# Kernel tuning notes

Hardware: AMD Instinct MI355X
Metric: run time of the kernel (lower is better)

The kernel has to match this reference:

```python
import jax, jax.numpy as jnp
import numpy as np

N_LAYERS, K, EPS = 3, 3, 1e-5
N, E, IN_CH, HID, OUT_CH = 50000, 800000, 16, 64, 4


def setup_inputs() -> dict:
    key = jax.random.key(0)
    ks = jax.random.split(key, 10)
    x = jax.random.normal(ks[0], (N, IN_CH), jnp.float32)
    edge_index = jax.random.randint(ks[1], (2, E), 0, N, dtype=jnp.int32)
    batch = jnp.zeros((N,), jnp.int32)  # unused by forward, kept for signature parity
    W_in = jax.random.normal(ks[2], (IN_CH, HID), jnp.float32) / np.sqrt(IN_CH)
    b_in = jnp.zeros((HID,), jnp.float32)
    cheb_W = jax.random.normal(ks[3], (N_LAYERS, K, HID, HID), jnp.float32) / np.sqrt(HID)
    cheb_b = jnp.zeros((N_LAYERS, HID), jnp.float32)
    ln_g = jnp.ones((N_LAYERS, HID), jnp.float32)
    ln_b = jnp.zeros((N_LAYERS, HID), jnp.float32)
    W_out = jax.random.normal(ks[4], (HID, OUT_CH), jnp.float32) / np.sqrt(HID)
    b_out = jnp.zeros((OUT_CH,), jnp.float32)
    return dict(x=x, edge_index=edge_index, batch=batch, W_in=W_in, b_in=b_in,
                cheb_W=cheb_W, cheb_b=cheb_b, ln_g=ln_g, ln_b=ln_b,
                W_out=W_out, b_out=b_out)


def _layernorm(h, g, b):
    mu = h.mean(-1, keepdims=True)
    var = ((h - mu) ** 2).mean(-1, keepdims=True)
    return (h - mu) * jax.lax.rsqrt(var + EPS) * g + b


def reference(x, edge_index, batch, W_in, b_in, cheb_W, cheb_b, ln_g, ln_b, W_out, b_out):
    n = x.shape[0]
    src, dst = edge_index[0], edge_index[1]
    # PyG ChebConv sym norm with lambda_max=2: L_hat = -D^{-1/2} A D^{-1/2}, zero diagonal
    deg = jax.ops.segment_sum(jnp.ones_like(src, x.dtype), src, num_segments=n)
    dinv = jnp.where(deg > 0, 1.0 / jnp.sqrt(jnp.maximum(deg, 1.0)), 0.0)
    w = -dinv[src] * dinv[dst]  # [E]

    def prop(h):  # h: [N, H] -> L_hat @ h via gather/scatter over edges
        return jax.ops.segment_sum(w[:, None] * h[src], dst, num_segments=n)

    h = x @ W_in + b_in
    for i in range(N_LAYERS):
        identity = h
        Tx0 = h
        out = Tx0 @ cheb_W[i, 0]
        Tx1 = prop(Tx0)
        out = out + Tx1 @ cheb_W[i, 1]
        for k in range(2, K):
            Tx2 = 2.0 * prop(Tx1) - Tx0
            out = out + Tx2 @ cheb_W[i, k]
            Tx0, Tx1 = Tx1, Tx2
        h = jax.nn.relu(out + cheb_b[i])  # dropout inactive (eval)
        h = h + identity
        h = _layernorm(h, ln_g[i], ln_b[i])
    return h @ W_out + b_out
```

## Files before the change

### kernel.cpp

```cpp
#include <hip/hip_runtime.h>
#include <hip/hip_bf16.h>

#define HID 64
#define CAP 64
#define LDK 200
#define Q4W 6272
typedef __hip_bfloat16 bf16;
typedef __attribute__((ext_vector_type(8))) short short8x;
typedef __attribute__((ext_vector_type(4))) float f32x4;

__device__ __forceinline__ float ldf(const void* p, int i, int bf) {
    return bf ? __bfloat162float(((const bf16*)p)[i]) : ((const float*)p)[i];
}
__device__ __forceinline__ unsigned short f2u16(float f) {
    bf16 h = __float2bfloat16(f);
    return *(unsigned short*)&h;
}
__device__ __forceinline__ float u162f(unsigned short u) {
    return __bfloat162float(*(const bf16*)&u);
}
__device__ __forceinline__ unsigned int pack2(float a, float b) {
    return (unsigned int)f2u16(a) | ((unsigned int)f2u16(b) << 16);
}
__device__ __forceinline__ unsigned int t3w(unsigned int t2w, unsigned int hw) {
    float a = 2.f * __uint_as_float(t2w << 16) - __uint_as_float(hw << 16);
    float b = 2.f * __uint_as_float(t2w & 0xffff0000u) - __uint_as_float(hw & 0xffff0000u);
    return pack2(a, b);
}
__device__ __forceinline__ void accum8(float* acc, uint4 r) {
    acc[0] += __uint_as_float(r.x << 16);
    acc[1] += __uint_as_float(r.x & 0xffff0000u);
    acc[2] += __uint_as_float(r.y << 16);
    acc[3] += __uint_as_float(r.y & 0xffff0000u);
    acc[4] += __uint_as_float(r.z << 16);
    acc[5] += __uint_as_float(r.z & 0xffff0000u);
    acc[6] += __uint_as_float(r.w << 16);
    acc[7] += __uint_as_float(r.w & 0xffff0000u);
}

__global__ __launch_bounds__(1024) void hist_both(const int* __restrict__ src,
                                                  const int* __restrict__ dst,
                                                  unsigned int* __restrict__ degS,
                                                  unsigned int* __restrict__ degD,
                                                  int E, int Q, int QW,
                                                  const unsigned short* __restrict__ lng,
                                                  int* __restrict__ flag,
                                                  bf16* __restrict__ HsPad,
                                                  bf16* __restrict__ T1sPad) {
    __shared__ unsigned int hs[Q4W];
    __shared__ unsigned int hd[Q4W];
    if (blockIdx.x == 0) {
        if (threadIdx.x == 0) *flag = (lng[0] == 0x3F80) ? 1 : 0;
        if (threadIdx.x < HID) {
            HsPad[threadIdx.x] = __float2bfloat16(0.f);
            T1sPad[threadIdx.x] = __float2bfloat16(0.f);
        }
    }
    int q = blockIdx.x & 3, sl = blockIdx.x >> 2;
    for (int i = threadIdx.x; i < QW; i += 1024) { hs[i] = 0u; hd[i] = 0u; }
    __syncthreads();
    int per = (E + 63) >> 6;
    int start = sl * per, end = min(start + per, E);
    int lo = q * Q;
    for (int e = start + threadIdx.x; e < end; e += 1024) {
        int s = src[e] - lo;
        int d = dst[e] - lo;
        if ((unsigned)s < (unsigned)Q) atomicAdd(&hs[s >> 1], (s & 1) ? 0x10000u : 1u);
        if ((unsigned)d < (unsigned)Q) atomicAdd(&hd[d >> 1], (d & 1) ? 0x10000u : 1u);
    }
    __syncthreads();
    unsigned int* os = degS + (size_t)blockIdx.x * QW;
    unsigned int* od = degD + (size_t)blockIdx.x * QW;
    for (int i = threadIdx.x; i < QW; i += 1024) { os[i] = hs[i]; od[i] = hd[i]; }
}

__global__ void prefix_prep(const unsigned int* __restrict__ degS,
                            const unsigned int* __restrict__ degD,
                            unsigned int* __restrict__ prefD,
                            float* __restrict__ dinv, int* __restrict__ cnts,
                            const void* __restrict__ chW, const int* __restrict__ flagp,
                            bf16* __restrict__ WT, int N, int Q, int QW, int dblkW) {
    int bid = blockIdx.x;
    if (bid < dblkW) {
        int wI = bid * 256 + threadIdx.x;
        if (wI < 4 * QW) {
            int q = wI / QW;
            int w = wI - q * QW;
            unsigned int run = 0, ss = 0;
            for (int sl = 0; sl < 64; ++sl) {
                size_t idx = (size_t)(sl * 4 + q) * QW + w;
                prefD[idx] = run;
                run += degD[idx];
                ss += degS[idx];
            }
            int n0 = q * Q + (w << 1);
            int d0 = (int)(ss & 0xffffu), d1 = (int)(ss >> 16);
            if (n0 < N) {
                dinv[n0] = (d0 > 0) ? 1.0f / sqrtf((float)d0) : 0.0f;
                cnts[n0] = (int)(run & 0xffffu);
            }
            if (((w << 1) + 1) < Q && (n0 + 1) < N) {
                dinv[n0 + 1] = (d1 > 0) ? 1.0f / sqrtf((float)d1) : 0.0f;
                cnts[n0 + 1] = (int)(run >> 16);
            }
        }
    } else {
        int bf = *flagp;
        int idx = (bid - dblkW) * 256 + threadIdx.x;
        if (idx < 3 * 64 * 192) {
            int L = idx / (64 * 192);
            int rem = idx % (64 * 192);
            int n = rem / 192;
            int k = rem % 192;
            int mat = k >> 6, r = k & 63;
            float v = ldf(chW, ((L * 3 + mat) * 64 + r) * 64 + n, bf);
            WT[idx] = __float2bfloat16(v);
        }
    }
}

__global__ __launch_bounds__(1024) void fill_input(
    const int* __restrict__ src, const int* __restrict__ dst,
    const unsigned int* __restrict__ prefD, unsigned short* __restrict__ srcsB,
    int E, int N, int Q, int QW,
    const void* __restrict__ x, const void* __restrict__ Win,
    const void* __restrict__ bin, const float* __restrict__ dinv,
    const int* __restrict__ flagp, bf16* __restrict__ H, bf16* __restrict__ Hs) {
    __shared__ unsigned int loc[Q4W];
    __shared__ float wsh[16 * HID];
    __shared__ float bb[HID];
    if (blockIdx.x < 256) {
        int q = blockIdx.x & 3, sl = blockIdx.x >> 2;
        const unsigned int* bp = prefD + (size_t)(sl * 4 + q) * QW;
        for (int i = threadIdx.x; i < QW; i += 1024) loc[i] = bp[i];
        __syncthreads();
        int per = (E + 63) >> 6;
        int start = sl * per, end = min(start + per, E);
        int lo = q * Q;
        for (int e = start + threadIdx.x; e < end; e += 1024) {
            int d = dst[e] - lo;
            if ((unsigned)d < (unsigned)Q) {
                unsigned int old = atomicAdd(&loc[d >> 1], (d & 1) ? 0x10000u : 1u);
                int slot = (int)((d & 1) ? (old >> 16) : (old & 0xffffu));
                if (slot < CAP) srcsB[(size_t)(lo + d) * CAP + slot] = (unsigned short)src[e];
            }
        }
        if (sl == 63) {
            __syncthreads();
            for (int i = threadIdx.x; i < QW; i += 1024) {
                unsigned int tot2 = loc[i];
                #pragma unroll
                for (int half = 0; half < 2; ++half) {
                    int d = (i << 1) + half;
                    int n = lo + d;
                    unsigned int tot = (half ? (tot2 >> 16) : tot2) & 0xffffu;
                    if (d < Q && n < N) {
                        int pe = min((int)((tot + 7u) & ~7u), CAP);
                        for (int s2 = (int)tot; s2 < pe; ++s2)
                            srcsB[(size_t)n * CAP + s2] = (unsigned short)N;
                    }
                }
            }
        }
    } else {
        int bf = *flagp;
        for (int i = threadIdx.x; i < 16 * HID; i += 1024) wsh[i] = ldf(Win, i, bf);
        if (threadIdx.x < HID) bb[threadIdx.x] = ldf(bin, threadIdx.x, bf);
        __syncthreads();
        int t = (blockIdx.x - 256) * 1024 + threadIdx.x;
        int n = t >> 6, j = t & 63;
        if (n >= N) return;
        float acc = bb[j];
        #pragma unroll
        for (int k = 0; k < 16; ++k) acc += ldf(x, n * 16 + k, bf) * wsh[k * HID + j];
        float dv = dinv[n];
        H[(size_t)n * HID + j] = __float2bfloat16(acc);
        Hs[(size_t)n * HID + j] = __float2bfloat16(acc * dv);
    }
}

__global__ __launch_bounds__(256) void prop8(const int* __restrict__ cnts,
                                             const unsigned short* __restrict__ srcsB,
                                             const float* __restrict__ dinv,
                                             const bf16* __restrict__ Hs,
                                             bf16* __restrict__ Tout,
                                             bf16* __restrict__ Touts,
                                             int N, int writeScaled) {
    int wid = blockIdx.x * 4 + (threadIdx.x >> 6);
    int lane = threadIdx.x & 63;
    int g8 = lane >> 3, sub = lane & 7;
    int node = wid * 8 + g8;
    bool vn = node < N;
    int nS = vn ? node : (N - 1);
    int cnt = vn ? min(cnts[nS], CAP) : 0;
    int mx = cnt;
    mx = max(mx, __shfl_xor(mx, 8, 64));
    mx = max(mx, __shfl_xor(mx, 16, 64));
    mx = max(mx, __shfl_xor(mx, 32, 64));
    int nblk = (mx + 7) >> 3;
    const unsigned short* bkt = srcsB + (size_t)nS * CAP;
    const unsigned short* HsU = (const unsigned short*)Hs;
    float acc[8] = {0.f, 0.f, 0.f, 0.f, 0.f, 0.f, 0.f, 0.f};

    uint4 rA[8], rB[8];
    auto issue = [&](uint4* r, int b) {
        uint4 iw = *(const uint4*)(bkt + b * 8);
        int id[8];
        id[0] = (int)(iw.x & 0xffffu); id[1] = (int)(iw.x >> 16);
        id[2] = (int)(iw.y & 0xffffu); id[3] = (int)(iw.y >> 16);
        id[4] = (int)(iw.z & 0xffffu); id[5] = (int)(iw.z >> 16);
        id[6] = (int)(iw.w & 0xffffu); id[7] = (int)(iw.w >> 16);
        int base = b * 8;
        #pragma unroll
        for (int k = 0; k < 8; ++k) {
            int idx = (base + k < cnt) ? id[k] : N;
            r[k] = *(const uint4*)(HsU + (size_t)idx * HID + sub * 8);
        }
    };
    auto acc8x = [&](uint4* r) {
        #pragma unroll
        for (int k = 0; k < 8; ++k) accum8(acc, r[k]);
    };

    if (nblk > 0) {
        issue(rA, 0);
        int b = 1;
        for (; b + 1 < nblk; b += 2) {
            issue(rB, b);
            acc8x(rA);
            issue(rA, b + 1);
            acc8x(rB);
        }
        if (b < nblk) { issue(rB, b); acc8x(rA); acc8x(rB); }
        else          { acc8x(rA); }
    }

    if (vn) {
        float dv = dinv[node];
        float t[8];
        #pragma unroll
        for (int k = 0; k < 8; ++k) t[k] = -dv * acc[k];
        uint4 o;
        o.x = pack2(t[0], t[1]); o.y = pack2(t[2], t[3]);
        o.z = pack2(t[4], t[5]); o.w = pack2(t[6], t[7]);
        *(uint4*)((unsigned short*)Tout + (size_t)node * HID + sub * 8) = o;
        if (writeScaled) {
            uint4 os;
            os.x = pack2(t[0] * dv, t[1] * dv); os.y = pack2(t[2] * dv, t[3] * dv);
            os.z = pack2(t[4] * dv, t[5] * dv); os.w = pack2(t[6] * dv, t[7] * dv);
            *(uint4*)((unsigned short*)Touts + (size_t)node * HID + sub * 8) = os;
        }
    }
}

__global__ __launch_bounds__(256) void fused_layer_mfma(
    bf16* __restrict__ H, bf16* __restrict__ Hs,
    const bf16* __restrict__ T1, const bf16* __restrict__ T2,
    const bf16* __restrict__ WT, const float* __restrict__ dinv,
    const void* __restrict__ cb, const void* __restrict__ g, const void* __restrict__ b,
    int voff, const int* __restrict__ flagp, int N, int ntiles,
    const void* __restrict__ Wout, const void* __restrict__ bout,
    void* __restrict__ yout, int lastL) {
    int bf = *flagp;
    __shared__ unsigned short Bs[64 * LDK];
    __shared__ unsigned short As[4][16 * LDK];
    __shared__ float woLds[HID * 4];
    __shared__ float boLds[4];
    int tid = threadIdx.x;
    const unsigned int* WT32 = (const unsigned int*)WT;
    for (int i = tid; i < 64 * 96; i += 256) {
        int row = i / 96, c2 = i % 96;
        *(unsigned int*)&Bs[row * LDK + c2 * 2] = WT32[i];
    }
    if (lastL) {
        for (int i = tid; i < HID * 4; i += 256) woLds[i] = ldf(Wout, i, bf);
        if (tid < 4) boLds[tid] = ldf(bout, tid, bf);
    }
    __syncthreads();

    int w = tid >> 6, lane = tid & 63;
    int q = lane >> 4, c = lane & 15;
    unsigned short* Aw = As[w];
    float cbv[4], gvv[4], bvv[4];
    #pragma unroll
    for (int b4 = 0; b4 < 4; ++b4) {
        cbv[b4] = ldf(cb, voff + b4 * 16 + c, bf);
        gvv[b4] = ldf(g,  voff + b4 * 16 + c, bf);
        bvv[b4] = ldf(b,  voff + b4 * 16 + c, bf);
    }

    for (int t = blockIdx.x * 4 + w; t < ntiles; t += gridDim.x * 4) {
        int base = t * 16;
        int srow = lane & 15;
        int node = base + srow;
        bool valid = node < N;
        uint4 h0 = {0,0,0,0}, h1 = {0,0,0,0}, a0 = {0,0,0,0}, a1 = {0,0,0,0};
        uint4 c0 = {0,0,0,0}, c1 = {0,0,0,0};
        if (valid) {
            const unsigned short* Hu  = (const unsigned short*)H  + (size_t)node * HID;
            const unsigned short* T1u = (const unsigned short*)T1 + (size_t)node * HID;
            const unsigned short* T2u = (const unsigned short*)T2 + (size_t)node * HID;
            h0 = *(const uint4*)(Hu + q * 8);
            h1 = *(const uint4*)(Hu + (4 + q) * 8);
            a0 = *(const uint4*)(T1u + q * 8);
            a1 = *(const uint4*)(T1u + (4 + q) * 8);
            c0 = *(const uint4*)(T2u + q * 8);
            c1 = *(const uint4*)(T2u + (4 + q) * 8);
        }
        uint4 t3a, t3b;
        t3a.x = t3w(c0.x, h0.x); t3a.y = t3w(c0.y, h0.y);
        t3a.z = t3w(c0.z, h0.z); t3a.w = t3w(c0.w, h0.w);
        t3b.x = t3w(c1.x, h1.x); t3b.y = t3w(c1.y, h1.y);
        t3b.z = t3w(c1.z, h1.z); t3b.w = t3w(c1.w, h1.w);
        unsigned short* Ar = &Aw[srow * LDK];
        *(uint4*)(Ar + q * 8)             = h0;
        *(uint4*)(Ar + (4 + q) * 8)       = h1;
        *(uint4*)(Ar + 64 + q * 8)        = a0;
        *(uint4*)(Ar + 64 + (4 + q) * 8)  = a1;
        *(uint4*)(Ar + 128 + q * 8)       = t3a;
        *(uint4*)(Ar + 128 + (4 + q) * 8) = t3b;

        f32x4 acc[4];
        #pragma unroll
        for (int b4 = 0; b4 < 4; ++b4) acc[b4] = (f32x4){0.f, 0.f, 0.f, 0.f};
        #pragma unroll
        for (int kk = 0; kk < 6; ++kk) {
            int kb = kk * 32 + q * 8;
            short8x af = *(const short8x*)&Aw[c * LDK + kb];
            #pragma unroll
            for (int b4 = 0; b4 < 4; ++b4) {
                short8x bfv = *(const short8x*)&Bs[(b4 * 16 + c) * LDK + kb];
                acc[b4] = __builtin_amdgcn_mfma_f32_16x16x32_bf16(af, bfv, acc[b4], 0, 0, 0);
            }
        }

        #pragma unroll
        for (int r = 0; r < 4; ++r) {
            int m = q * 4 + r;
            int nd = base + m;
            float vv[4];
            float s = 0.f, s2 = 0.f;
            #pragma unroll
            for (int b4 = 0; b4 < 4; ++b4) {
                float hval = u162f(Aw[m * LDK + b4 * 16 + c]);
                float o = acc[b4][r] + cbv[b4];
                float tv = fmaxf(o, 0.f) + hval;
                vv[b4] = tv;
                s += tv; s2 += tv * tv;
            }
            #pragma unroll
            for (int msk = 1; msk < 16; msk <<= 1) {
                s  += __shfl_xor(s,  msk, 64);
                s2 += __shfl_xor(s2, msk, 64);
            }
            float mu = s * (1.f / 64.f);
            float var = s2 * (1.f / 64.f) - mu * mu;
            float rs = rsqrtf(var + 1e-5f);
            if (!lastL) {
                if (nd < N) {
                    float dvn = dinv[nd];
                    #pragma unroll
                    for (int b4 = 0; b4 < 4; ++b4) {
                        float hn = (vv[b4] - mu) * rs * gvv[b4] + bvv[b4];
                        H[(size_t)nd * HID + b4 * 16 + c]  = __float2bfloat16(hn);
                        Hs[(size_t)nd * HID + b4 * 16 + c] = __float2bfloat16(hn * dvn);
                    }
                }
            } else {
                float ya0 = 0.f, ya1 = 0.f, ya2 = 0.f, ya3 = 0.f;
                #pragma unroll
                for (int b4 = 0; b4 < 4; ++b4) {
                    float hn = (nd < N) ? (vv[b4] - mu) * rs * gvv[b4] + bvv[b4] : 0.f;
                    const float* wr = &woLds[(b4 * 16 + c) * 4];
                    ya0 += hn * wr[0]; ya1 += hn * wr[1];
                    ya2 += hn * wr[2]; ya3 += hn * wr[3];
                }
                #pragma unroll
                for (int msk = 1; msk < 16; msk <<= 1) {
                    ya0 += __shfl_xor(ya0, msk, 64);
                    ya1 += __shfl_xor(ya1, msk, 64);
                    ya2 += __shfl_xor(ya2, msk, 64);
                    ya3 += __shfl_xor(ya3, msk, 64);
                }
                if (c == 0 && nd < N) {
                    ya0 += boLds[0]; ya1 += boLds[1];
                    ya2 += boLds[2]; ya3 += boLds[3];
                    if (bf) {
                        uint2 o;
                        o.x = pack2(ya0, ya1); o.y = pack2(ya2, ya3);
                        *(uint2*)((unsigned short*)yout + (size_t)nd * 4) = o;
                    } else {
                        float4 o = {ya0, ya1, ya2, ya3};
                        *(float4*)((float*)yout + (size_t)nd * 4) = o;
                    }
                }
            }
        }
    }
}

extern "C" void kernel_launch(void* const* d_in, const int* in_sizes, int n_in,
                              void* d_out, int out_size, void* d_ws, size_t ws_size,
                              hipStream_t stream) {
    const void* x    = d_in[0];
    const int*  ei   = (const int*)d_in[1];
    const void* Win  = d_in[3];
    const void* bin  = d_in[4];
    const void* chW  = d_in[5];
    const void* chb  = d_in[6];
    const void* lng  = d_in[7];
    const void* lnb  = d_in[8];
    const void* Wout = d_in[9];
    const void* bout = d_in[10];

    int N = in_sizes[0] / 16;
    int E = in_sizes[1] / 2;
    const int* src = ei;
    const int* dst = ei + E;
    int ntiles = (N + 15) / 16;
    int Q = (N + 3) / 4;
    int QW = (Q + 1) / 2;
    int dblkW = (4 * QW + 255) / 256;
    int inBlocks = (N * 64 + 1023) / 1024;
    int fusedBlocks = (ntiles + 3) / 4;
    int propBlocks = (N + 31) / 32;

    char* p = (char*)d_ws;
    auto carve = [&](size_t bytes) {
        char* r = p;
        p += (bytes + 255) & ~(size_t)255;
        return r;
    };
    int*            flag  = (int*)carve(256);
    float*          dinv  = (float*)carve((size_t)N * 4);
    int*            cnts  = (int*)carve((size_t)N * 4);
    unsigned short* srcsB = (unsigned short*)carve((size_t)N * CAP * 2);
    bf16*           WT    = (bf16*)carve((size_t)3 * 64 * 192 * 2);
    bf16*           H     = (bf16*)carve((size_t)N * HID * 2);
    bf16*           Hs    = (bf16*)carve((size_t)(N + 1) * HID * 2);
    bf16*           T1    = (bf16*)carve((size_t)N * HID * 2);
    bf16*           T1s   = (bf16*)carve((size_t)(N + 1) * HID * 2);
    bf16*           T2    = (bf16*)carve((size_t)N * HID * 2);
    unsigned int*   degS  = (unsigned int*)carve((size_t)256 * QW * 4);
    unsigned int*   degD  = (unsigned int*)carve((size_t)256 * QW * 4);
    unsigned int*   prefD = (unsigned int*)carve((size_t)256 * QW * 4);

    hipLaunchKernelGGL(hist_both, dim3(256), dim3(1024), 0, stream,
                       src, dst, degS, degD, E, Q, QW,
                       (const unsigned short*)lng, flag,
                       Hs + (size_t)N * HID, T1s + (size_t)N * HID);
    hipLaunchKernelGGL(prefix_prep, dim3(dblkW + 144), dim3(256), 0, stream,
                       degS, degD, prefD, dinv, cnts, chW, flag, WT, N, Q, QW, dblkW);
    hipLaunchKernelGGL(fill_input, dim3(256 + inBlocks), dim3(1024), 0, stream,
                       src, dst, prefD, srcsB, E, N, Q, QW,
                       x, Win, bin, dinv, flag, H, Hs);

    for (int L = 0; L < 3; ++L) {
        hipLaunchKernelGGL(prop8, dim3(propBlocks), dim3(256), 0, stream,
                           cnts, srcsB, dinv, Hs, T1, T1s, N, 1);
        hipLaunchKernelGGL(prop8, dim3(propBlocks), dim3(256), 0, stream,
                           cnts, srcsB, dinv, T1s, T2, (bf16*)0, N, 0);
        hipLaunchKernelGGL(fused_layer_mfma, dim3(fusedBlocks), dim3(256), 0, stream,
                           H, Hs, T1, T2, WT + (size_t)L * 64 * 192, dinv,
                           chb, lng, lnb, L * HID, flag, N, ntiles,
                           Wout, bout, d_out, (L == 2) ? 1 : 0);
    }
}
```

Measured before the change: 254.5 us.

## Fuse second Chebyshev propagation into the per-layer MFMA kernel

The second sparse propagation (T2 = L_hat @ T1) now runs inside the fused layer kernel instead of a separate prop8 launch. Each wave gathers neighbour rows of T1s for its 16-node tile and writes the result straight into the LDS A-tile, so the T2 buffer is never written to or read from global memory. This saves one launch per layer and the T2 round trip through memory. In exchange the fused kernel does irregular gathers inside its tile loop, which may raise register pressure and make the MFMA part wait on gather latency.

```diff
diff --git a/kernel.cpp b/kernel.cpp
--- a/kernel.cpp
+++ b/kernel.cpp
@@ -255,7 +255,8 @@
 
 __global__ __launch_bounds__(256) void fused_layer_mfma(
     bf16* __restrict__ H, bf16* __restrict__ Hs,
-    const bf16* __restrict__ T1, const bf16* __restrict__ T2,
+    const bf16* __restrict__ T1, const bf16* __restrict__ T1s,
+    const int* __restrict__ cnts, const unsigned short* __restrict__ srcsB,
     const bf16* __restrict__ WT, const float* __restrict__ dinv,
     const void* __restrict__ cb, const void* __restrict__ g, const void* __restrict__ b,
     int voff, const int* __restrict__ flagp, int N, int ntiles,
@@ -280,7 +281,9 @@
 
     int w = tid >> 6, lane = tid & 63;
     int q = lane >> 4, c = lane & 15;
+    int g8 = lane >> 3, sub8 = lane & 7;
     unsigned short* Aw = As[w];
+    const unsigned short* TsU = (const unsigned short*)T1s;
     float cbv[4], gvv[4], bvv[4];
     #pragma unroll
     for (int b4 = 0; b4 < 4; ++b4) {
@@ -291,28 +294,63 @@
 
     for (int t = blockIdx.x * 4 + w; t < ntiles; t += gridDim.x * 4) {
         int base = t * 16;
+
+        #pragma unroll
+        for (int hh = 0; hh < 2; ++hh) {
+            int nloc = hh * 8 + g8;
+            int nodeG = base + nloc;
+            bool vg = nodeG < N;
+            int nSg = vg ? nodeG : (N - 1);
+            int cntg = vg ? min(cnts[nSg], CAP) : 0;
+            int mxg = cntg;
+            mxg = max(mxg, __shfl_xor(mxg, 8, 64));
+            mxg = max(mxg, __shfl_xor(mxg, 16, 64));
+            mxg = max(mxg, __shfl_xor(mxg, 32, 64));
+            const unsigned short* bkt = srcsB + (size_t)nSg * CAP;
+            float acg[8] = {0.f, 0.f, 0.f, 0.f, 0.f, 0.f, 0.f, 0.f};
+            for (int nb0 = 0; nb0 < mxg; nb0 += 8) {
+                uint4 iw = *(const uint4*)(bkt + nb0);
+                int id[8];
+                id[0] = (int)(iw.x & 0xffffu); id[1] = (int)(iw.x >> 16);
+                id[2] = (int)(iw.y & 0xffffu); id[3] = (int)(iw.y >> 16);
+                id[4] = (int)(iw.z & 0xffffu); id[5] = (int)(iw.z >> 16);
+                id[6] = (int)(iw.w & 0xffffu); id[7] = (int)(iw.w >> 16);
+                #pragma unroll
+                for (int k = 0; k < 8; ++k) {
+                    int idx = (nb0 + k < cntg) ? id[k] : N;
+                    uint4 r = *(const uint4*)(TsU + (size_t)idx * HID + sub8 * 8);
+                    accum8(acg, r);
+                }
+            }
+            float dvg = vg ? dinv[nSg] : 0.f;
+            uint4 o;
+            o.x = pack2(-dvg * acg[0], -dvg * acg[1]);
+            o.y = pack2(-dvg * acg[2], -dvg * acg[3]);
+            o.z = pack2(-dvg * acg[4], -dvg * acg[5]);
+            o.w = pack2(-dvg * acg[6], -dvg * acg[7]);
+            *(uint4*)&Aw[nloc * LDK + 128 + sub8 * 8] = o;
+        }
+
         int srow = lane & 15;
         int node = base + srow;
         bool valid = node < N;
         uint4 h0 = {0,0,0,0}, h1 = {0,0,0,0}, a0 = {0,0,0,0}, a1 = {0,0,0,0};
-        uint4 c0 = {0,0,0,0}, c1 = {0,0,0,0};
         if (valid) {
             const unsigned short* Hu  = (const unsigned short*)H  + (size_t)node * HID;
             const unsigned short* T1u = (const unsigned short*)T1 + (size_t)node * HID;
-            const unsigned short* T2u = (const unsigned short*)T2 + (size_t)node * HID;
             h0 = *(const uint4*)(Hu + q * 8);
             h1 = *(const uint4*)(Hu + (4 + q) * 8);
             a0 = *(const uint4*)(T1u + q * 8);
             a1 = *(const uint4*)(T1u + (4 + q) * 8);
-            c0 = *(const uint4*)(T2u + q * 8);
-            c1 = *(const uint4*)(T2u + (4 + q) * 8);
-        }
+        }
+        unsigned short* Ar = &Aw[srow * LDK];
+        uint4 c0 = *(const uint4*)(Ar + 128 + q * 8);
+        uint4 c1 = *(const uint4*)(Ar + 128 + (4 + q) * 8);
         uint4 t3a, t3b;
         t3a.x = t3w(c0.x, h0.x); t3a.y = t3w(c0.y, h0.y);
         t3a.z = t3w(c0.z, h0.z); t3a.w = t3w(c0.w, h0.w);
         t3b.x = t3w(c1.x, h1.x); t3b.y = t3w(c1.y, h1.y);
         t3b.z = t3w(c1.z, h1.z); t3b.w = t3w(c1.w, h1.w);
-        unsigned short* Ar = &Aw[srow * LDK];
         *(uint4*)(Ar + q * 8)             = h0;
         *(uint4*)(Ar + (4 + q) * 8)       = h1;
         *(uint4*)(Ar + 64 + q * 8)        = a0;
@@ -440,7 +478,6 @@
     bf16*           Hs    = (bf16*)carve((size_t)(N + 1) * HID * 2);
     bf16*           T1    = (bf16*)carve((size_t)N * HID * 2);
     bf16*           T1s   = (bf16*)carve((size_t)(N + 1) * HID * 2);
-    bf16*           T2    = (bf16*)carve((size_t)N * HID * 2);
     unsigned int*   degS  = (unsigned int*)carve((size_t)256 * QW * 4);
     unsigned int*   degD  = (unsigned int*)carve((size_t)256 * QW * 4);
     unsigned int*   prefD = (unsigned int*)carve((size_t)256 * QW * 4);
@@ -458,10 +495,9 @@
     for (int L = 0; L < 3; ++L) {
         hipLaunchKernelGGL(prop8, dim3(propBlocks), dim3(256), 0, stream,
                            cnts, srcsB, dinv, Hs, T1, T1s, N, 1);
-        hipLaunchKernelGGL(prop8, dim3(propBlocks), dim3(256), 0, stream,
-                           cnts, srcsB, dinv, T1s, T2, (bf16*)0, N, 0);
         hipLaunchKernelGGL(fused_layer_mfma, dim3(fusedBlocks), dim3(256), 0, stream,
-                           H, Hs, T1, T2, WT + (size_t)L * 64 * 192, dinv,
+                           H, Hs, T1, T1s, cnts, srcsB,
+                           WT + (size_t)L * 64 * 192, dinv,
                            chb, lng, lnb, L * HID, flag, N, ntiles,
                            Wout, bout, d_out, (L == 2) ? 1 : 0);
     }
```

Result: no change. 256.9 us (+0.9%).
